# Optimization experiments

Measured on AMD Instinct MI355X. Metric: run time of the kernel, lower is better.

Reference implementation:

```python
import jax, jax.numpy as jnp
import numpy as np
from math import sqrt

B, T, D = 32, 65536, 512
NPOS, NTIME = 8192, 2048


def setup_inputs() -> dict:
    key = jax.random.key(0)
    rng = np.random.default_rng(0)
    # jagged lengths summing exactly to T
    raw = rng.integers(256, 4096, size=B).astype(np.float64)
    lengths = np.floor(raw / raw.sum() * T).astype(np.int64)
    lengths[-1] += T - lengths.sum()
    offsets = np.concatenate([[0], np.cumsum(lengths)]).astype(np.int64)
    # monotonically increasing timestamps (positive per-token deltas)
    deltas = rng.integers(1, 1000, size=T).astype(np.int64)
    timestamps = np.cumsum(deltas)
    # number of target items per sequence (strictly less than length)
    num_targets = np.minimum(rng.integers(0, 32, size=B), lengths // 2).astype(np.int64)
    k1, k2, k3 = jax.random.split(key, 3)
    seq_embeddings = jax.random.normal(k1, (T, D), dtype=jnp.float32)
    bp = sqrt(1.0 / NPOS)
    bt = sqrt(1.0 / NTIME)
    pos_emb = jax.random.uniform(k2, (NPOS, D), minval=-bp, maxval=bp, dtype=jnp.float32)
    ts_emb = jax.random.uniform(k3, (NTIME + 1, D), minval=-bt, maxval=bt, dtype=jnp.float32)
    return {
        "max_seq_len": 4096,
        "seq_lengths": jnp.asarray(lengths),
        "seq_offsets": jnp.asarray(offsets),
        "seq_embeddings": seq_embeddings,
        "num_targets": jnp.asarray(num_targets),
        "seq_timestamps": jnp.asarray(timestamps),
        "pos_emb": pos_emb,
        "ts_emb": ts_emb,
    }


def reference(max_seq_len, seq_lengths, seq_offsets, seq_embeddings, num_targets, seq_timestamps, pos_emb, ts_emb):
    T_, D_ = seq_embeddings.shape
    alpha = float(D_) ** 0.5
    max_pos_ind = pos_emb.shape[0]
    max_ts_ind = ts_emb.shape[0] - 1  # num_time_buckets

    tok = jnp.arange(T_)
    # sequence id per flat token via offsets (offsets[0]=0, offsets[B]=T)
    seq_id = jnp.searchsorted(seq_offsets, tok, side="right") - 1
    local = tok - seq_offsets[seq_id]                 # position within sequence
    L = seq_lengths[seq_id]

    # position bucket: targets share the position of the first target
    high = L - num_targets[seq_id]                    # interleave_targets=False
    high = jnp.minimum(high, max_pos_ind - 1)         # clamp to table size
    pos = jnp.clip(jnp.minimum(local, high), 0, max_pos_ind - 1)

    # time bucket: sqrt of delta to the sequence's last (query) timestamp
    query_ts = seq_timestamps[seq_offsets[seq_id] + L - 1]
    delta = jnp.maximum(query_ts - seq_timestamps, 0).astype(jnp.float32)
    bucket = jnp.floor(jnp.sqrt(delta)).astype(jnp.int32)
    bucket = jnp.clip(bucket, 0, max_ts_ind)

    # fused gather + scale + add
    return seq_embeddings * alpha + pos_emb[pos] + ts_emb[bucket]
```

## Files before the change

kernel.cpp:

```cpp
#include <hip/hip_runtime.h>
#include <math.h>

typedef float f32x4 __attribute__((ext_vector_type(4)));

__global__ void hstu_meta_kernel(const int* __restrict__ seq_lengths,
                                 const int* __restrict__ seq_offsets,
                                 const int* __restrict__ num_targets,
                                 const int* __restrict__ seq_timestamps,
                                 int2* __restrict__ meta,
                                 int T, int B, int NPOS, int NTIME) {
    int t = blockIdx.x * blockDim.x + threadIdx.x;
    if (t >= T) return;

    int lo = 0, hi = B;
    while (hi - lo > 1) {
        int mid = (lo + hi) >> 1;
        if (seq_offsets[mid] <= t) lo = mid; else hi = mid;
    }
    const int sid   = lo;
    const int off   = seq_offsets[sid];
    const int L     = seq_lengths[sid];
    const int local = t - off;

    int high = L - num_targets[sid];
    if (high > NPOS - 1) high = NPOS - 1;
    int pos = local < high ? local : high;
    if (pos < 0) pos = 0;
    if (pos > NPOS - 1) pos = NPOS - 1;

    const int qts   = seq_timestamps[off + L - 1];
    int delta = qts - seq_timestamps[t];
    if (delta < 0) delta = 0;
    int bucket = (int)floorf(sqrtf((float)delta));
    if (bucket < 0) bucket = 0;
    if (bucket > NTIME) bucket = NTIME;

    meta[t] = make_int2(pos, bucket);
}

template <int C4S>
__global__ void __launch_bounds__(256)
hstu_fuse_wave_row(const f32x4* __restrict__ emb,
                   const f32x4* __restrict__ pos_emb,
                   const f32x4* __restrict__ ts_emb,
                   const int2* __restrict__ meta,
                   f32x4* __restrict__ out,
                   int T, float alpha) {
    constexpr int C4   = 1 << C4S;
    constexpr int F4PL = C4 >> 6;
    static_assert(F4PL >= 1, "row must span at least one float4 per lane");

    const int lane = threadIdx.x & 63;
    const int wpb  = blockDim.x >> 6;
    const int nw   = gridDim.x * wpb;
    int t = blockIdx.x * wpb + (threadIdx.x >> 6);
    if (t >= T) return;

    int2 m = meta[t];
    while (true) {
        const int tn = t + nw;
        int2 mn = m;
        if (tn < T) mn = meta[tn];

        const f32x4* ep = emb     + (((size_t)t)   << C4S) + lane;
        const f32x4* pp = pos_emb + (((size_t)m.x) << C4S) + lane;
        const f32x4* tp = ts_emb  + (((size_t)m.y) << C4S) + lane;

        f32x4 e[F4PL], p[F4PL], q[F4PL];
#pragma unroll
        for (int j = 0; j < F4PL; ++j) e[j] = __builtin_nontemporal_load(ep + 64 * j);
#pragma unroll
        for (int j = 0; j < F4PL; ++j) p[j] = pp[64 * j];
#pragma unroll
        for (int j = 0; j < F4PL; ++j) q[j] = tp[64 * j];

        f32x4* op = out + (((size_t)t) << C4S) + lane;
#pragma unroll
        for (int j = 0; j < F4PL; ++j) {
            f32x4 o;
            o.x = fmaf(e[j].x, alpha, p[j].x + q[j].x);
            o.y = fmaf(e[j].y, alpha, p[j].y + q[j].y);
            o.z = fmaf(e[j].z, alpha, p[j].z + q[j].z);
            o.w = fmaf(e[j].w, alpha, p[j].w + q[j].w);
            __builtin_nontemporal_store(o, op + 64 * j);
        }

        if (tn >= T) break;
        t = tn;
        m = mn;
    }
}

__global__ void __launch_bounds__(256)
hstu_fuse_kernel_gen(const f32x4* __restrict__ emb,
                     const f32x4* __restrict__ pos_emb,
                     const f32x4* __restrict__ ts_emb,
                     const int2* __restrict__ meta,
                     f32x4* __restrict__ out,
                     int total4, int c4, float alpha) {
    const int stride = gridDim.x * blockDim.x;
    for (int idx = blockIdx.x * blockDim.x + threadIdx.x; idx < total4; idx += stride) {
        const int t = idx / c4;
        const int c = idx - t * c4;
        const int2 m = meta[t];
        const f32x4 e  = emb[idx];
        const f32x4 pe = pos_emb[(size_t)m.x * c4 + c];
        const f32x4 te = ts_emb[(size_t)m.y * c4 + c];
        f32x4 o;
        o.x = fmaf(e.x, alpha, pe.x + te.x);
        o.y = fmaf(e.y, alpha, pe.y + te.y);
        o.z = fmaf(e.z, alpha, pe.z + te.z);
        o.w = fmaf(e.w, alpha, pe.w + te.w);
        out[idx] = o;
    }
}

extern "C" void kernel_launch(void* const* d_in, const int* in_sizes, int n_in,
                              void* d_out, int out_size, void* d_ws, size_t ws_size,
                              hipStream_t stream) {
    const int* seq_lengths    = (const int*)d_in[1];
    const int* seq_offsets    = (const int*)d_in[2];
    const float* seq_emb      = (const float*)d_in[3];
    const int* num_targets    = (const int*)d_in[4];
    const int* seq_timestamps = (const int*)d_in[5];
    const float* pos_emb      = (const float*)d_in[6];
    const float* ts_emb       = (const float*)d_in[7];
    float* out                = (float*)d_out;

    const int B     = in_sizes[1];
    const int T     = in_sizes[5];
    const int D     = in_sizes[3] / T;
    const int NPOS  = in_sizes[6] / D;
    const int NTIME = in_sizes[7] / D - 1;
    const float alpha = sqrtf((float)D);

    int2* meta = (int2*)d_ws;

    {
        const int block = 256;
        const int grid  = (T + block - 1) / block;
        hstu_meta_kernel<<<grid, block, 0, stream>>>(
            seq_lengths, seq_offsets, num_targets, seq_timestamps,
            meta, T, B, NPOS, NTIME);
    }

    const int c4 = D / 4;
    const int block = 256;
    const int wpb = block / 64;

    if (c4 == 128 || c4 == 64 || c4 == 256) {
        int grid = (T + wpb - 1) / wpb;
        if (grid > 2048) grid = 2048;
        if (c4 == 128) {
            hstu_fuse_wave_row<7><<<grid, block, 0, stream>>>(
                (const f32x4*)seq_emb, (const f32x4*)pos_emb, (const f32x4*)ts_emb,
                meta, (f32x4*)out, T, alpha);
        } else if (c4 == 64) {
            hstu_fuse_wave_row<6><<<grid, block, 0, stream>>>(
                (const f32x4*)seq_emb, (const f32x4*)pos_emb, (const f32x4*)ts_emb,
                meta, (f32x4*)out, T, alpha);
        } else {
            hstu_fuse_wave_row<8><<<grid, block, 0, stream>>>(
                (const f32x4*)seq_emb, (const f32x4*)pos_emb, (const f32x4*)ts_emb,
                meta, (f32x4*)out, T, alpha);
        }
    } else {
        const long total4l = (long)T * c4;
        const int total4 = (int)total4l;
        int grid = (int)((total4l + block - 1) / block);
        if (grid > 2048) grid = 2048;
        hstu_fuse_kernel_gen<<<grid, block, 0, stream>>>(
            (const f32x4*)seq_emb, (const f32x4*)pos_emb, (const f32x4*)ts_emb,
            meta, (f32x4*)out, total4, c4, alpha);
    }
}
```

Measured before the change: 261.0 us.

## Assign contiguous row chunks per wave with XCD-aware block swizzle

Replaces the grid-stride loop with a launch where each wave handles 8 consecutive rows. The grid now covers all rows instead of being capped at 2048 blocks. Block indices are remapped so that each group of blocks dispatched to the same XCD (assuming round-robin over 8) works on a contiguous range of rows. This aims to improve L2 locality for the pos_emb rows that consecutive tokens share and for the streaming accesses. The cost is many more blocks and an assumption about how blocks are dispatched across chiplets.

```diff
diff --git a/kernel.cpp b/kernel.cpp
--- a/kernel.cpp
+++ b/kernel.cpp
@@ -38,29 +38,33 @@
     meta[t] = make_int2(pos, bucket);
 }
 
-template <int C4S>
+template <int C4S, int RPW>
 __global__ void __launch_bounds__(256)
-hstu_fuse_wave_row(const f32x4* __restrict__ emb,
-                   const f32x4* __restrict__ pos_emb,
-                   const f32x4* __restrict__ ts_emb,
-                   const int2* __restrict__ meta,
-                   f32x4* __restrict__ out,
-                   int T, float alpha) {
+hstu_fuse_rows(const f32x4* __restrict__ emb,
+               const f32x4* __restrict__ pos_emb,
+               const f32x4* __restrict__ ts_emb,
+               const int2* __restrict__ meta,
+               f32x4* __restrict__ out,
+               int T, float alpha) {
     constexpr int C4   = 1 << C4S;
     constexpr int F4PL = C4 >> 6;
     static_assert(F4PL >= 1, "row must span at least one float4 per lane");
 
+    const int cpx = gridDim.x >> 3;
+    const int sw  = (blockIdx.x & 7) * cpx + (blockIdx.x >> 3);
+
     const int lane = threadIdx.x & 63;
     const int wpb  = blockDim.x >> 6;
-    const int nw   = gridDim.x * wpb;
-    int t = blockIdx.x * wpb + (threadIdx.x >> 6);
-    if (t >= T) return;
+    const int w    = sw * wpb + (threadIdx.x >> 6);
+    const int t0   = w * RPW;
+    if (t0 >= T) return;
+    const int tend = (t0 + RPW < T) ? (t0 + RPW) : T;
 
-    int2 m = meta[t];
-    while (true) {
-        const int tn = t + nw;
+    int2 m = meta[t0];
+    for (int t = t0; t < tend; ++t) {
+        const int tn = t + 1;
         int2 mn = m;
-        if (tn < T) mn = meta[tn];
+        if (tn < tend) mn = meta[tn];
 
         const f32x4* ep = emb     + (((size_t)t)   << C4S) + lane;
         const f32x4* pp = pos_emb + (((size_t)m.x) << C4S) + lane;
@@ -85,8 +89,6 @@
             __builtin_nontemporal_store(o, op + 64 * j);
         }
 
-        if (tn >= T) break;
-        t = tn;
         m = mn;
     }
 }
@@ -147,20 +149,21 @@
     const int c4 = D / 4;
     const int block = 256;
     const int wpb = block / 64;
+    const int RPW = 8;
 
     if (c4 == 128 || c4 == 64 || c4 == 256) {
-        int grid = (T + wpb - 1) / wpb;
-        if (grid > 2048) grid = 2048;
+        int grid = (T + wpb * RPW - 1) / (wpb * RPW);
+        grid = ((grid + 7) / 8) * 8;
         if (c4 == 128) {
-            hstu_fuse_wave_row<7><<<grid, block, 0, stream>>>(
+            hstu_fuse_rows<7, 8><<<grid, block, 0, stream>>>(
                 (const f32x4*)seq_emb, (const f32x4*)pos_emb, (const f32x4*)ts_emb,
                 meta, (f32x4*)out, T, alpha);
         } else if (c4 == 64) {
-            hstu_fuse_wave_row<6><<<grid, block, 0, stream>>>(
+            hstu_fuse_rows<6, 8><<<grid, block, 0, stream>>>(
                 (const f32x4*)seq_emb, (const f32x4*)pos_emb, (const f32x4*)ts_emb,
                 meta, (f32x4*)out, T, alpha);
         } else {
-            hstu_fuse_wave_row<8><<<grid, block, 0, stream>>>(
+            hstu_fuse_rows<8, 8><<<grid, block, 0, stream>>>(
                 (const f32x4*)seq_emb, (const f32x4*)pos_emb, (const f32x4*)ts_emb,
                 meta, (f32x4*)out, T, alpha);
         }
```

After: 275.9 us. 5.7% more time.

## Partition tokens by position residue per XCD and gather from bf16 tables

Applied to the files above, without the earlier changes.

Adds a fused kernel for D=512 that assigns tokens to block groups by local position mod 8. With round-robin block placement, each XCD's L2 then sees only a slice of the position table. The pos and ts tables are also converted to bf16 in workspace on every call, which halves the bytes gathered per row. The conversion costs extra kernel launches and memory traffic, and the bf16 tables lose precision in the added embeddings. Each block also does a serial prefix over B sequences plus a binary search per token.

```diff
diff --git a/kernel.cpp b/kernel.cpp
--- a/kernel.cpp
+++ b/kernel.cpp
@@ -2,6 +2,29 @@
 #include <math.h>
 
 typedef float f32x4 __attribute__((ext_vector_type(4)));
+typedef unsigned int u32x4 __attribute__((ext_vector_type(4)));
+typedef unsigned short u16x4 __attribute__((ext_vector_type(4)));
+typedef unsigned short u16x8 __attribute__((ext_vector_type(8)));
+
+__device__ __forceinline__ float bf2f(unsigned short u) {
+    union { unsigned int i; float f; } v;
+    v.i = ((unsigned int)u) << 16;
+    return v.f;
+}
+
+__global__ void __launch_bounds__(256)
+hstu_cvt_bf16(const u32x4* __restrict__ src, u16x4* __restrict__ dst, int n4) {
+    int i = blockIdx.x * blockDim.x + threadIdx.x;
+    const int stride = gridDim.x * blockDim.x;
+    for (; i < n4; i += stride) {
+        u32x4 u = src[i];
+        u16x4 r;
+#pragma unroll
+        for (int j = 0; j < 4; ++j)
+            r[j] = (unsigned short)((u[j] + 0x7FFFu + ((u[j] >> 16) & 1u)) >> 16);
+        dst[i] = r;
+    }
+}
 
 __global__ void hstu_meta_kernel(const int* __restrict__ seq_lengths,
                                  const int* __restrict__ seq_offsets,
@@ -36,6 +59,75 @@
     if (bucket > NTIME) bucket = NTIME;
 
     meta[t] = make_int2(pos, bucket);
+}
+
+__global__ void __launch_bounds__(256)
+hstu_fuse_mod8_d512(const f32x4* __restrict__ emb,
+                    const unsigned short* __restrict__ pos_bf,
+                    const unsigned short* __restrict__ ts_bf,
+                    const int2* __restrict__ meta,
+                    const int* __restrict__ seq_lengths,
+                    const int* __restrict__ seq_offsets,
+                    f32x4* __restrict__ out,
+                    int B, float alpha) {
+    constexpr int D = 512;
+    __shared__ int sC[129];
+    __shared__ int sOff[128];
+
+    const int x = blockIdx.x & 7;
+
+    if (threadIdx.x == 0) {
+        int c = 0;
+        sC[0] = 0;
+        for (int s = 0; s < B; ++s) {
+            const int L = seq_lengths[s];
+            const int cnt = (L > x) ? ((L - 1 - x) / 8 + 1) : 0;
+            c += cnt;
+            sC[s + 1] = c;
+        }
+    }
+    if ((int)threadIdx.x < B) sOff[threadIdx.x] = seq_offsets[threadIdx.x];
+    __syncthreads();
+
+    const int Nx   = sC[B];
+    const int lane = threadIdx.x & 63;
+    const int wpb  = blockDim.x >> 6;
+    const int W    = (gridDim.x >> 3) * wpb;
+    const int wv   = (blockIdx.x >> 3) * wpb + (threadIdx.x >> 6);
+
+    for (int k = wv; k < Nx; k += W) {
+        int lo = 0, hi = B;
+        while (hi - lo > 1) {
+            int mid = (lo + hi) >> 1;
+            if (sC[mid] <= k) lo = mid; else hi = mid;
+        }
+        const int s     = lo;
+        const int local = x + 8 * (k - sC[s]);
+        const int t     = sOff[s] + local;
+
+        const int2 m = meta[t];
+
+        const f32x4* ep = emb + (((size_t)t) << 7) + lane * 2;
+        const f32x4 e0 = __builtin_nontemporal_load(ep);
+        const f32x4 e1 = __builtin_nontemporal_load(ep + 1);
+
+        const u16x8 pv = *((const u16x8*)(pos_bf + ((size_t)m.x) * D) + lane);
+        const u16x8 tv = *((const u16x8*)(ts_bf  + ((size_t)m.y) * D) + lane);
+
+        f32x4 o0, o1;
+        o0.x = fmaf(e0.x, alpha, bf2f(pv[0]) + bf2f(tv[0]));
+        o0.y = fmaf(e0.y, alpha, bf2f(pv[1]) + bf2f(tv[1]));
+        o0.z = fmaf(e0.z, alpha, bf2f(pv[2]) + bf2f(tv[2]));
+        o0.w = fmaf(e0.w, alpha, bf2f(pv[3]) + bf2f(tv[3]));
+        o1.x = fmaf(e1.x, alpha, bf2f(pv[4]) + bf2f(tv[4]));
+        o1.y = fmaf(e1.y, alpha, bf2f(pv[5]) + bf2f(tv[5]));
+        o1.z = fmaf(e1.z, alpha, bf2f(pv[6]) + bf2f(tv[6]));
+        o1.w = fmaf(e1.w, alpha, bf2f(pv[7]) + bf2f(tv[7]));
+
+        f32x4* op = out + (((size_t)t) << 7) + lane * 2;
+        __builtin_nontemporal_store(o0, op);
+        __builtin_nontemporal_store(o1, op + 1);
+    }
 }
 
 template <int C4S>
@@ -134,6 +226,12 @@
     const int NTIME = in_sizes[7] / D - 1;
     const float alpha = sqrtf((float)D);
 
+    const size_t metaBytes = (((size_t)T * 8) + 15) & ~(size_t)15;
+    const size_t posBytes  = (((size_t)NPOS * D * 2) + 15) & ~(size_t)15;
+    const size_t tsBytes   = (size_t)(NTIME + 1) * D * 2;
+    const bool mod8_ok = (D == 512) && (B >= 1) && (B <= 128) &&
+                         (ws_size >= metaBytes + posBytes + tsBytes);
+
     int2* meta = (int2*)d_ws;
 
     {
@@ -142,6 +240,25 @@
         hstu_meta_kernel<<<grid, block, 0, stream>>>(
             seq_lengths, seq_offsets, num_targets, seq_timestamps,
             meta, T, B, NPOS, NTIME);
+    }
+
+    if (mod8_ok) {
+        unsigned short* pos_bf = (unsigned short*)((char*)d_ws + metaBytes);
+        unsigned short* ts_bf  = (unsigned short*)((char*)d_ws + metaBytes + posBytes);
+
+        {
+            const int n4p = NPOS * D / 4;
+            const int n4t = (NTIME + 1) * D / 4;
+            hstu_cvt_bf16<<<512, 256, 0, stream>>>(
+                (const u32x4*)pos_emb, (u16x4*)pos_bf, n4p);
+            hstu_cvt_bf16<<<256, 256, 0, stream>>>(
+                (const u32x4*)ts_emb, (u16x4*)ts_bf, n4t);
+        }
+
+        hstu_fuse_mod8_d512<<<2048, 256, 0, stream>>>(
+            (const f32x4*)seq_emb, pos_bf, ts_bf, meta,
+            seq_lengths, seq_offsets, (f32x4*)out, B, alpha);
+        return;
     }
 
     const int c4 = D / 4;
```

Result: slower. 279.8 us (+7.2%).

## Quantize position and timestamp tables to uint8 before the fused gather-add

Applied to the files above, without the earlier changes.

Adds per-call kernels that find the absolute maximum of the position and time embedding tables and quantize them to offset uint8 into workspace. A new D=512 fused kernel gathers 8 bytes per lane from each quantized table instead of 32 bytes and dequantizes with FMAs. The goal is to cut gather bandwidth on the table reads. In exchange it adds five extra launches plus a full read and write of both tables on every call, and it introduces quantization error in the table contributions.

```diff
diff --git a/kernel.cpp b/kernel.cpp
--- a/kernel.cpp
+++ b/kernel.cpp
@@ -2,6 +2,46 @@
 #include <math.h>
 
 typedef float f32x4 __attribute__((ext_vector_type(4)));
+typedef unsigned int u32x2 __attribute__((ext_vector_type(2)));
+typedef unsigned int u32x4 __attribute__((ext_vector_type(4)));
+
+__global__ void hstu_init_scales(unsigned int* sc) {
+    if (threadIdx.x < 2 && blockIdx.x == 0) sc[threadIdx.x] = 0u;
+}
+
+__global__ void __launch_bounds__(256)
+hstu_absmax(const f32x4* __restrict__ src, int n4, unsigned int* __restrict__ sc) {
+    float m = 0.f;
+    const int stride = gridDim.x * blockDim.x;
+    for (int i = blockIdx.x * blockDim.x + threadIdx.x; i < n4; i += stride) {
+        f32x4 v = src[i];
+        m = fmaxf(m, fmaxf(fmaxf(fabsf(v.x), fabsf(v.y)), fmaxf(fabsf(v.z), fabsf(v.w))));
+    }
+#pragma unroll
+    for (int off = 32; off; off >>= 1) m = fmaxf(m, __shfl_xor(m, off));
+    if ((threadIdx.x & 63) == 0) atomicMax(sc, __float_as_uint(m));
+}
+
+__global__ void __launch_bounds__(256)
+hstu_quant_u8(const f32x4* __restrict__ src, u32x4* __restrict__ dst, int n16,
+              const unsigned int* __restrict__ sc) {
+    const float am  = __uint_as_float(*sc);
+    const float inv = am > 0.f ? 127.0f / am : 0.f;
+    const int stride = gridDim.x * blockDim.x;
+    for (int i = blockIdx.x * blockDim.x + threadIdx.x; i < n16; i += stride) {
+        u32x4 r;
+#pragma unroll
+        for (int j = 0; j < 4; ++j) {
+            f32x4 v = src[i * 4 + j];
+            unsigned q0 = (unsigned)(__float2int_rn(v.x * inv) + 128);
+            unsigned q1 = (unsigned)(__float2int_rn(v.y * inv) + 128);
+            unsigned q2 = (unsigned)(__float2int_rn(v.z * inv) + 128);
+            unsigned q3 = (unsigned)(__float2int_rn(v.w * inv) + 128);
+            r[j] = q0 | (q1 << 8) | (q2 << 16) | (q3 << 24);
+        }
+        dst[i] = r;
+    }
+}
 
 __global__ void hstu_meta_kernel(const int* __restrict__ seq_lengths,
                                  const int* __restrict__ seq_offsets,
@@ -36,6 +76,57 @@
     if (bucket > NTIME) bucket = NTIME;
 
     meta[t] = make_int2(pos, bucket);
+}
+
+__global__ void __launch_bounds__(256)
+hstu_fuse_u8_d512(const f32x4* __restrict__ emb,
+                  const unsigned char* __restrict__ pos_q,
+                  const unsigned char* __restrict__ ts_q,
+                  const int2* __restrict__ meta,
+                  const unsigned int* __restrict__ scales,
+                  f32x4* __restrict__ out,
+                  int T, float alpha) {
+    const float sp = __uint_as_float(scales[0]) * (1.0f / 127.0f);
+    const float st = __uint_as_float(scales[1]) * (1.0f / 127.0f);
+    const float C  = -128.0f * (sp + st);
+
+    const int lane = threadIdx.x & 63;
+    const int wpb  = blockDim.x >> 6;
+    const int nw   = gridDim.x * wpb;
+    int t = blockIdx.x * wpb + (threadIdx.x >> 6);
+    if (t >= T) return;
+
+    int2 m = meta[t];
+    while (true) {
+        const int tn = t + nw;
+        int2 mn = m;
+        if (tn < T) mn = meta[tn];
+
+        const f32x4* ep = emb + (((size_t)t) << 7) + lane * 2;
+        const f32x4 e0 = __builtin_nontemporal_load(ep);
+        const f32x4 e1 = __builtin_nontemporal_load(ep + 1);
+
+        const u32x2 pq = *(const u32x2*)(pos_q + ((size_t)m.x << 9) + lane * 8);
+        const u32x2 tq = *(const u32x2*)(ts_q  + ((size_t)m.y << 9) + lane * 8);
+
+        f32x4 o0, o1;
+        o0.x = fmaf(e0.x, alpha, fmaf((float)( pq[0]        & 0xffu), sp, fmaf((float)( tq[0]        & 0xffu), st, C)));
+        o0.y = fmaf(e0.y, alpha, fmaf((float)((pq[0] >>  8) & 0xffu), sp, fmaf((float)((tq[0] >>  8) & 0xffu), st, C)));
+        o0.z = fmaf(e0.z, alpha, fmaf((float)((pq[0] >> 16) & 0xffu), sp, fmaf((float)((tq[0] >> 16) & 0xffu), st, C)));
+        o0.w = fmaf(e0.w, alpha, fmaf((float)((pq[0] >> 24) & 0xffu), sp, fmaf((float)((tq[0] >> 24) & 0xffu), st, C)));
+        o1.x = fmaf(e1.x, alpha, fmaf((float)( pq[1]        & 0xffu), sp, fmaf((float)( tq[1]        & 0xffu), st, C)));
+        o1.y = fmaf(e1.y, alpha, fmaf((float)((pq[1] >>  8) & 0xffu), sp, fmaf((float)((tq[1] >>  8) & 0xffu), st, C)));
+        o1.z = fmaf(e1.z, alpha, fmaf((float)((pq[1] >> 16) & 0xffu), sp, fmaf((float)((tq[1] >> 16) & 0xffu), st, C)));
+        o1.w = fmaf(e1.w, alpha, fmaf((float)((pq[1] >> 24) & 0xffu), sp, fmaf((float)((tq[1] >> 24) & 0xffu), st, C)));
+
+        f32x4* op = out + (((size_t)t) << 7) + lane * 2;
+        __builtin_nontemporal_store(o0, op);
+        __builtin_nontemporal_store(o1, op + 1);
+
+        if (tn >= T) break;
+        t = tn;
+        m = mn;
+    }
 }
 
 template <int C4S>
@@ -134,7 +225,15 @@
     const int NTIME = in_sizes[7] / D - 1;
     const float alpha = sqrtf((float)D);
 
-    int2* meta = (int2*)d_ws;
+    const size_t scBytes   = 16;
+    const size_t metaBytes = (((size_t)T * 8) + 15) & ~(size_t)15;
+    const size_t posBytes  = (((size_t)NPOS * D) + 15) & ~(size_t)15;
+    const size_t tsBytes   = (size_t)(NTIME + 1) * D;
+    const bool u8_ok = (D == 512) && (NPOS % 16 == 0) && ((NTIME + 1) % 16 == 0) &&
+                       (ws_size >= scBytes + metaBytes + posBytes + tsBytes);
+
+    unsigned int* scales = (unsigned int*)d_ws;
+    int2* meta = (int2*)((char*)d_ws + scBytes);
 
     {
         const int block = 256;
@@ -142,6 +241,28 @@
         hstu_meta_kernel<<<grid, block, 0, stream>>>(
             seq_lengths, seq_offsets, num_targets, seq_timestamps,
             meta, T, B, NPOS, NTIME);
+    }
+
+    if (u8_ok) {
+        unsigned char* pos_q = (unsigned char*)d_ws + scBytes + metaBytes;
+        unsigned char* ts_q  = pos_q + posBytes;
+
+        hstu_init_scales<<<1, 64, 0, stream>>>(scales);
+        hstu_absmax<<<1024, 256, 0, stream>>>((const f32x4*)pos_emb, NPOS * D / 4, scales);
+        hstu_absmax<<<512, 256, 0, stream>>>((const f32x4*)ts_emb, (NTIME + 1) * D / 4, scales + 1);
+        hstu_quant_u8<<<1024, 256, 0, stream>>>((const f32x4*)pos_emb, (u32x4*)pos_q,
+                                                NPOS * D / 16, scales);
+        hstu_quant_u8<<<512, 256, 0, stream>>>((const f32x4*)ts_emb, (u32x4*)ts_q,
+                                               (NTIME + 1) * D / 16, scales + 1);
+
+        const int block = 256;
+        const int wpb = block / 64;
+        int grid = (T + wpb - 1) / wpb;
+        if (grid > 2048) grid = 2048;
+        hstu_fuse_u8_d512<<<grid, block, 0, stream>>>(
+            (const f32x4*)seq_emb, pos_q, ts_q, meta, scales,
+            (f32x4*)out, T, alpha);
+        return;
     }
 
     const int c4 = D / 4;
```

New measurement: 259.4 us. About the same (-0.6%).
